# Kernel tuning notes

Measured on AMD Instinct MI355X. Metric: run time of the kernel, lower is better.

## Reference

```python
import jax, jax.numpy as jnp
import numpy as np

B, T, TRAIN = 4, 2048, 1536
D, H, L, FF, V = 512, 8, 12, 2048, 100
DH = D // H
ROPE_BASE = 100000.0


def layer_norm(x, g, b, eps=1e-5):
    mu = jnp.mean(x, axis=-1, keepdims=True)
    var = jnp.mean(jnp.square(x - mu), axis=-1, keepdims=True)
    return (x - mu) * jax.lax.rsqrt(var + eps) * g + b


def rope_cos_sin(t, dh):
    inv_freq = 1.0 / (ROPE_BASE ** (jnp.arange(0, dh, 2, dtype=jnp.float32) / dh))  # (dh/2,)
    ang = jnp.arange(t, dtype=jnp.float32)[:, None] * inv_freq[None, :]  # (T, dh/2)
    return jnp.cos(ang), jnp.sin(ang)


def apply_rope_interleaved(x, cos, sin):
    # x: (B, T, H, DH); interleaved pairs (x0,x1),(x2,x3),...
    x1, x2 = x[..., 0::2], x[..., 1::2]
    c, s = cos[None, :, None, :], sin[None, :, None, :]
    r1 = x1 * c - x2 * s
    r2 = x1 * s + x2 * c
    return jnp.stack([r1, r2], axis=-1).reshape(x.shape)


def setup_inputs() -> dict:
    key = jax.random.key(0)
    ks = jax.random.split(key, 20)
    sc = 0.02
    inp = {
        'R': jax.random.normal(ks[0], (B, T, D), jnp.float32),
        'y_train': jax.random.randint(ks[1], (B, TRAIN), 0, V),
        'emb': jax.random.normal(ks[2], (V, D), jnp.float32) * sc,
        'Wqkv': jax.random.normal(ks[3], (L, D, 3 * D), jnp.float32) * sc,
        'bqkv': jnp.zeros((L, 3 * D), jnp.float32),
        'Wo': jax.random.normal(ks[4], (L, D, D), jnp.float32) * sc,
        'bo': jnp.zeros((L, D), jnp.float32),
        'ln1_g': jnp.ones((L, D), jnp.float32),
        'ln1_b': jnp.zeros((L, D), jnp.float32),
        'ln2_g': jnp.ones((L, D), jnp.float32),
        'ln2_b': jnp.zeros((L, D), jnp.float32),
        'W1': jax.random.normal(ks[5], (L, D, FF), jnp.float32) * sc,
        'b1': jnp.zeros((L, FF), jnp.float32),
        'W2': jax.random.normal(ks[6], (L, FF, D), jnp.float32) * sc,
        'b2': jnp.zeros((L, D), jnp.float32),
        'pW1': jax.random.normal(ks[7], (D, 2 * D), jnp.float32) * sc,
        'pb1': jnp.zeros((2 * D,), jnp.float32),
        'pW2': jax.random.normal(ks[8], (2 * D, V), jnp.float32) * sc,
        'pb2': jnp.zeros((V,), jnp.float32),
    }
    return inp


def icl_forward(R, y_train, emb, Wqkv, bqkv, Wo, bo, ln1_g, ln1_b, ln2_g, ln2_b, W1, b1, W2, b2, pW1, pb1, pW2, pb2):
    b, t, d = R.shape
    train = y_train.shape[1]
    # label embedding: train rows get emb[y], test rows get zeros
    y_emb = jnp.concatenate([emb[y_train], jnp.zeros((b, t - train, d), R.dtype)], axis=1)
    rep = R + y_emb
    # ICL mask: column j visible iff j < train or j == i
    idx = jnp.arange(t)
    allowed = (idx[None, :] < train) | (idx[:, None] == idx[None, :])
    mask = jnp.where(allowed, 0.0, -jnp.inf).astype(R.dtype)  # (T, T)
    cos, sin = rope_cos_sin(t, DH)
    scale = 1.0 / jnp.sqrt(jnp.asarray(DH, R.dtype))

    def block(x, p):
        wqkv, bq, wo, bob, g1, be1, g2, be2, w1, bb1, w2, bb2 = p
        h = layer_norm(x, g1, be1)
        qkv = h @ wqkv + bq  # (B,T,3D)
        q, k, v = jnp.split(qkv, 3, axis=-1)
        q = q.reshape(b, t, H, DH)
        k = k.reshape(b, t, H, DH)
        v = v.reshape(b, t, H, DH)
        q = apply_rope_interleaved(q, cos, sin)
        k = apply_rope_interleaved(k, cos, sin)
        scores = jnp.einsum('bthd,bshd->bhts', q, k) * scale + mask
        attn = jax.nn.softmax(scores, axis=-1)
        o = jnp.einsum('bhts,bshd->bthd', attn, v).reshape(b, t, d)
        x = x + o @ wo + bob
        h2 = layer_norm(x, g2, be2)
        x = x + jax.nn.gelu(h2 @ w1 + bb1) @ w2 + bb2
        return x, None

    rep, _ = jax.lax.scan(block, rep, (Wqkv, bqkv, Wo, bo, ln1_g, ln1_b, ln2_g, ln2_b, W1, b1, W2, b2))
    test = rep[:, train:, :]
    logits = jax.nn.gelu(test @ pW1 + pb1) @ pW2 + pb2  # (B, test, V)
    return logits


def reference(R, y_train, emb, Wqkv, bqkv, Wo, bo, ln1_g, ln1_b, ln2_g, ln2_b, W1, b1, W2, b2, pW1, pb1, pW2, pb2):
    return icl_forward(R, y_train, emb, Wqkv, bqkv, Wo, bo, ln1_g, ln1_b, ln2_g, ln2_b, W1, b1, W2, b2, pW1, pb1, pW2, pb2)
```

## Files before the change

kernel.cpp:

```cpp
#include <hip/hip_runtime.h>
#include <hip/hip_bf16.h>

#define BB 4
#define TT 2048
#define TRAIN 1536
#define DD 512
#define HH 8
#define LL 12
#define FFD 2048
#define VV 100
#define DH 64
#define NT (BB*TT)
#define NTEST (BB*(TT-TRAIN))

typedef __bf16 bf16x8 __attribute__((ext_vector_type(8)));
typedef float  f32x4  __attribute__((ext_vector_type(4)));

#define GLDS16(g, l) __builtin_amdgcn_global_load_lds( \
    (const __attribute__((address_space(1))) void*)(g), \
    (__attribute__((address_space(3))) void*)(l), 16, 0, 0)

__global__ __launch_bounds__(256) void emb_add(const float* __restrict__ R,
                                               const int* __restrict__ y,
                                               const float* __restrict__ emb,
                                               float* __restrict__ rep) {
    int idx = blockIdx.x * 256 + threadIdx.x;
    int d = idx & 511;
    int n = idx >> 9;
    int t = n & (TT - 1);
    int b = n >> 11;
    float val = R[idx];
    if (t < TRAIN) {
        int tok = y[b * TRAIN + t];
        val += emb[(size_t)tok * DD + d];
    }
    rep[idx] = val;
}

__global__ __launch_bounds__(256) void ln_wave(const float* __restrict__ x,
                                               const float* __restrict__ g,
                                               const float* __restrict__ bta,
                                               __bf16* __restrict__ out) {
    int row = blockIdx.x * 4 + (threadIdx.x >> 6);
    int lane = threadIdx.x & 63;
    const float* xr = x + (size_t)row * DD + lane * 8;
    float4 a = *(const float4*)xr;
    float4 c = *(const float4*)(xr + 4);
    float s  = a.x + a.y + a.z + a.w + c.x + c.y + c.z + c.w;
    float sq = a.x*a.x + a.y*a.y + a.z*a.z + a.w*a.w + c.x*c.x + c.y*c.y + c.z*c.z + c.w*c.w;
#pragma unroll
    for (int off = 1; off < 64; off <<= 1) {
        s  += __shfl_xor(s, off);
        sq += __shfl_xor(sq, off);
    }
    float mu  = s * (1.0f / DD);
    float var = sq * (1.0f / DD) - mu * mu;
    float inv = rsqrtf(var + 1e-5f);
    const float* gp = g + lane * 8;
    const float* bp = bta + lane * 8;
    float4 g0 = *(const float4*)gp, g1 = *(const float4*)(gp + 4);
    float4 b0 = *(const float4*)bp, b1 = *(const float4*)(bp + 4);
    __bf16 o8[8];
    o8[0] = (__bf16)((a.x - mu) * inv * g0.x + b0.x);
    o8[1] = (__bf16)((a.y - mu) * inv * g0.y + b0.y);
    o8[2] = (__bf16)((a.z - mu) * inv * g0.z + b0.z);
    o8[3] = (__bf16)((a.w - mu) * inv * g0.w + b0.w);
    o8[4] = (__bf16)((c.x - mu) * inv * g1.x + b1.x);
    o8[5] = (__bf16)((c.y - mu) * inv * g1.y + b1.y);
    o8[6] = (__bf16)((c.z - mu) * inv * g1.z + b1.z);
    o8[7] = (__bf16)((c.w - mu) * inv * g1.w + b1.w);
    *(uint4*)(out + (size_t)row * DD + lane * 8) = *(uint4*)o8;
}

__global__ __launch_bounds__(256) void rope_tab(float* __restrict__ ctab, float* __restrict__ stab) {
    int idx = blockIdx.x * 256 + threadIdx.x;
    int p = idx & 31, t = idx >> 5;
    double freq = exp(-((double)(2 * p) / 64.0) * log(100000.0));
    double ang = (double)t * freq;
    ctab[idx] = (float)cos(ang);
    stab[idx] = (float)sin(ang);
}

__global__ __launch_bounds__(256) void rope_vt(const __bf16* __restrict__ qkv,
                                               const float* __restrict__ ctab,
                                               const float* __restrict__ stab,
                                               __bf16* __restrict__ qo,
                                               __bf16* __restrict__ ko,
                                               __bf16* __restrict__ vt) {
    int bh = blockIdx.y; int b = bh >> 3, h = bh & 7;
    int t0 = blockIdx.x * 64;
    __shared__ __bf16 tile[64][72];
    int tid = threadIdx.x;
    {
        int r = tid >> 2, cg = (tid & 3) * 16;
        const __bf16* src = qkv + (size_t)(b * TT + t0 + r) * (3 * DD) + 2 * DD + h * DH + cg;
        *(uint4*)&tile[r][cg]     = *(const uint4*)&src[0];
        *(uint4*)&tile[r][cg + 8] = *(const uint4*)&src[8];
    }
#pragma unroll
    for (int c = 0; c < 8; ++c) {
        int pidx = c * 256 + tid;
        int tl = pidx >> 5, p = pidx & 31;
        int t = t0 + tl;
        const __bf16* base = qkv + (size_t)(b * TT + t) * (3 * DD) + h * DH;
        float co = ctab[t * 32 + p], si = stab[t * 32 + p];
        float x1 = (float)base[2 * p],       x2 = (float)base[2 * p + 1];
        float k1 = (float)base[DD + 2 * p], k2 = (float)base[DD + 2 * p + 1];
        size_t ob = ((size_t)bh * TT + t) * DH;
        qo[ob + 2 * p]     = (__bf16)(x1 * co - x2 * si);
        qo[ob + 2 * p + 1] = (__bf16)(x1 * si + x2 * co);
        ko[ob + 2 * p]     = (__bf16)(k1 * co - k2 * si);
        ko[ob + 2 * p + 1] = (__bf16)(k1 * si + k2 * co);
    }
    __syncthreads();
    {
        int dh = tid >> 2, tg = (tid & 3) * 16;
        __bf16 outv[16];
#pragma unroll
        for (int j = 0; j < 16; ++j) outv[j] = tile[tg + j][dh];
        __bf16* dst = vt + ((size_t)bh * DH + dh) * TT + t0 + tg;
        *(uint4*)&dst[0] = *(uint4*)&outv[0];
        *(uint4*)&dst[8] = *(uint4*)&outv[8];
    }
}

#define NCH (TRAIN/128)
#define PSE 136

__global__ __launch_bounds__(512, 2) void attn_mfma(const __bf16* __restrict__ q,
                                                    const __bf16* __restrict__ k,
                                                    const __bf16* __restrict__ vt,
                                                    __bf16* __restrict__ obuf) {
    __shared__ __align__(16) __bf16 Kb[2][128 * 64];
    __shared__ __align__(16) __bf16 Vb[64 * 128];
    __shared__ __align__(16) __bf16 Pb[256 * PSE];
    __shared__ float sself[256];

    const int tid = threadIdx.x;
    const int bh = blockIdx.y;
    const int b = bh >> 3, hh = bh & 7;
    const size_t kbase = (size_t)bh * TT * DH;
    const int t0q = blockIdx.x * 256;
    const int w = tid >> 6;
    const int lane = tid & 63;
    const int l16 = lane & 15;
    const int quad = lane >> 4;
    const int x7 = l16 & 7;

    bf16x8 qa[2][2];
#pragma unroll
    for (int mi = 0; mi < 2; ++mi)
#pragma unroll
        for (int ks = 0; ks < 2; ++ks) {
            const __bf16* qg = q + kbase + (size_t)(t0q + w * 32 + mi * 16 + l16) * DH + ks * 32 + quad * 8;
            uint4 u = *(const uint4*)qg;
            const __bf16* pb = (const __bf16*)&u;
            bf16x8 vq;
#pragma unroll
            for (int j = 0; j < 8; ++j) vq[j] = (__bf16)((float)pb[j] * 0.125f);
            qa[mi][ks] = vq;
        }

    const int krl = lane >> 3, ksl = lane & 7;
    const int vrl = lane >> 4, vsl = lane & 15;

    f32x4 oa[2][4] = {};
    float lsum[2] = {0.f, 0.f};

    {
        const __bf16* g = k + kbase;
#pragma unroll
        for (int c = 0; c < 2; ++c) {
            int rb = w * 2 + c;
            GLDS16(g + (size_t)(rb * 8 + krl) * DH + ((ksl ^ krl) * 8), &Kb[0][rb * 512]);
        }
    }

    for (int ci = 0; ci < NCH; ++ci) {
        __syncthreads();
        {
#pragma unroll
            for (int c = 0; c < 2; ++c) {
                int rb = w * 2 + c;
                int dh = rb * 4 + vrl;
                GLDS16(vt + kbase + (size_t)dh * TT + ci * 128 + ((vsl ^ (dh & 7)) * 8), &Vb[rb * 512]);
            }
        }

        const __bf16* kc = Kb[ci & 1];
        f32x4 acc[2][8] = {};
        __builtin_amdgcn_s_setprio(1);
#pragma unroll
        for (int ks = 0; ks < 2; ++ks) {
            bf16x8 kf[8];
#pragma unroll
            for (int ni = 0; ni < 8; ++ni)
                kf[ni] = *(const bf16x8*)&kc[(ni * 16 + l16) * 64 + (((ks * 4 + quad) ^ x7) * 8)];
#pragma unroll
            for (int ni = 0; ni < 8; ++ni) {
                acc[0][ni] = __builtin_amdgcn_mfma_f32_16x16x32_bf16(kf[ni], qa[0][ks], acc[0][ni], 0, 0, 0);
                acc[1][ni] = __builtin_amdgcn_mfma_f32_16x16x32_bf16(kf[ni], qa[1][ks], acc[1][ni], 0, 0, 0);
            }
        }
        __builtin_amdgcn_s_setprio(0);

#pragma unroll
        for (int mi = 0; mi < 2; ++mi) {
            float rs = 0.f;
#pragma unroll
            for (int ni = 0; ni < 8; ++ni) {
                float p0 = __expf(acc[mi][ni][0]);
                float p1 = __expf(acc[mi][ni][1]);
                float p2 = __expf(acc[mi][ni][2]);
                float p3 = __expf(acc[mi][ni][3]);
                rs += (p0 + p1) + (p2 + p3);
                __bf16 p4[4] = {(__bf16)p0, (__bf16)p1, (__bf16)p2, (__bf16)p3};
                *(uint2*)&Pb[(w * 32 + mi * 16 + l16) * PSE + ni * 16 + quad * 4] = *(const uint2*)p4;
            }
            rs += __shfl_xor(rs, 16);
            rs += __shfl_xor(rs, 32);
            lsum[mi] += rs;
        }

        __syncthreads();
        if (ci + 1 < NCH) {
            const __bf16* g = k + kbase + (size_t)((ci + 1) * 128) * DH;
            __bf16* dst = Kb[(ci + 1) & 1];
#pragma unroll
            for (int c = 0; c < 2; ++c) {
                int rb = w * 2 + c;
                GLDS16(g + (size_t)(rb * 8 + krl) * DH + ((ksl ^ krl) * 8), dst + rb * 512);
            }
        }

        __builtin_amdgcn_s_setprio(1);
#pragma unroll
        for (int ks = 0; ks < 4; ++ks) {
            bf16x8 vf[4];
#pragma unroll
            for (int ni = 0; ni < 4; ++ni)
                vf[ni] = *(const bf16x8*)&Vb[(ni * 16 + l16) * 128 + (((ks * 4 + quad) ^ x7) * 8)];
            bf16x8 pa0 = *(const bf16x8*)&Pb[(w * 32 + l16) * PSE + ks * 32 + quad * 8];
            bf16x8 pa1 = *(const bf16x8*)&Pb[(w * 32 + 16 + l16) * PSE + ks * 32 + quad * 8];
#pragma unroll
            for (int ni = 0; ni < 4; ++ni) {
                oa[0][ni] = __builtin_amdgcn_mfma_f32_16x16x32_bf16(pa0, vf[ni], oa[0][ni], 0, 0, 0);
                oa[1][ni] = __builtin_amdgcn_mfma_f32_16x16x32_bf16(pa1, vf[ni], oa[1][ni], 0, 0, 0);
            }
        }
        __builtin_amdgcn_s_setprio(0);
    }

    float lr[2][4];
#pragma unroll
    for (int mi = 0; mi < 2; ++mi)
#pragma unroll
        for (int r = 0; r < 4; ++r)
            lr[mi][r] = __shfl(lsum[mi], quad * 4 + r);

    if (t0q >= TRAIN) {
        __bf16* selfV = &Kb[0][0];
        __syncthreads();
        {
            int dh = tid >> 3, c0 = (tid & 7) * 32;
            const __bf16* vg = vt + kbase + (size_t)dh * TT + t0q + c0;
#pragma unroll
            for (int u = 0; u < 4; ++u)
                *(uint4*)&selfV[dh * 256 + c0 + u * 8] = *(const uint4*)&vg[u * 8];
            int row = tid >> 1, hf = tid & 1;
            const __bf16* qp = q + kbase + (size_t)(t0q + row) * DH + hf * 32;
            const __bf16* kp = k + kbase + (size_t)(t0q + row) * DH + hf * 32;
            float dacc = 0.f;
#pragma unroll
            for (int u = 0; u < 4; ++u) {
                uint4 uq = *(const uint4*)&qp[u * 8];
                uint4 uk = *(const uint4*)&kp[u * 8];
                const __bf16* pq = (const __bf16*)&uq;
                const __bf16* pk = (const __bf16*)&uk;
#pragma unroll
                for (int j = 0; j < 8; ++j) dacc += (float)pq[j] * (float)pk[j];
            }
            dacc += __shfl_xor(dacc, 1);
            sself[row] = dacc * 0.125f;
        }
        __syncthreads();
#pragma unroll
        for (int mi = 0; mi < 2; ++mi)
#pragma unroll
            for (int r = 0; r < 4; ++r) {
                int qr = w * 32 + mi * 16 + quad * 4 + r;
                float pp = __expf(sself[qr]);
                lr[mi][r] += pp;
#pragma unroll
                for (int ni = 0; ni < 4; ++ni)
                    oa[mi][ni][r] += pp * (float)selfV[(ni * 16 + l16) * 256 + qr];
            }
    }

#pragma unroll
    for (int mi = 0; mi < 2; ++mi)
#pragma unroll
        for (int r = 0; r < 4; ++r) {
            float inv = 1.f / lr[mi][r];
            int trow = t0q + w * 32 + mi * 16 + quad * 4 + r;
            __bf16* op = obuf + ((size_t)(b * TT) + trow) * DD + hh * 64;
#pragma unroll
            for (int ni = 0; ni < 4; ++ni)
                op[ni * 16 + l16] = (__bf16)(oa[mi][ni][r] * inv);
        }
}

__global__ __launch_bounds__(256) void transpose_pad(const float* __restrict__ src,
                                                     __bf16* __restrict__ dst,
                                                     int K, int N) {
    __shared__ __bf16 t[32][33];
    int n0 = blockIdx.x * 32, k0 = blockIdx.y * 32;
    int tx = threadIdx.x & 31, ty = threadIdx.x >> 5;
#pragma unroll
    for (int i = 0; i < 4; ++i) {
        int nn = n0 + tx;
        t[ty + i * 8][tx] = (nn < N) ? (__bf16)src[(size_t)(k0 + ty + i * 8) * N + nn] : (__bf16)0.f;
    }
    __syncthreads();
#pragma unroll
    for (int i = 0; i < 4; ++i) {
        dst[(size_t)(n0 + ty + i * 8) * K + k0 + tx] = t[tx][ty + i * 8];
    }
}

__global__ __launch_bounds__(256) void transpose_all(const float* __restrict__ s0,
                                                     const float* __restrict__ s1,
                                                     const float* __restrict__ s2,
                                                     const float* __restrict__ s3,
                                                     __bf16* __restrict__ d0, __bf16* __restrict__ d1,
                                                     __bf16* __restrict__ d2, __bf16* __restrict__ d3) {
    int i = blockIdx.x;
    const float* src; __bf16* dst; int K, N, tx, ty;
    if (i < 768)       { src = s0; dst = d0; K = 512;  N = 1536; int j = i;        tx = j % 48; ty = j / 48; }
    else if (i < 1024) { src = s1; dst = d1; K = 512;  N = 512;  int j = i - 768;  tx = j % 16; ty = j / 16; }
    else if (i < 2048) { src = s2; dst = d2; K = 512;  N = 2048; int j = i - 1024; tx = j % 64; ty = j / 64; }
    else               { src = s3; dst = d3; K = 2048; N = 512;  int j = i - 2048; tx = j % 16; ty = j / 16; }
    __shared__ __bf16 t[32][33];
    int n0 = tx * 32, k0 = ty * 32;
    int lx = threadIdx.x & 31, ly = threadIdx.x >> 5;
#pragma unroll
    for (int c = 0; c < 4; ++c)
        t[ly + c * 8][lx] = (__bf16)src[(size_t)(k0 + ly + c * 8) * N + n0 + lx];
    __syncthreads();
#pragma unroll
    for (int c = 0; c < 4; ++c)
        dst[(size_t)(n0 + ly + c * 8) * K + k0 + lx] = t[lx][ly + c * 8];
}

template <int EP, int TN>
__global__ __launch_bounds__(256) void gemm_bt(const __bf16* __restrict__ A,
                                               const __bf16* __restrict__ Bt,
                                               const float* __restrict__ bias,
                                               float* __restrict__ resid,
                                               __bf16* __restrict__ Cout,
                                               int M, int N, int K) {
    constexpr int NI = TN / 32;
    __shared__ __align__(16) __bf16 As[2][128 * 32];
    __shared__ __align__(16) __bf16 Bs[2][TN * 32];
    const int tid = threadIdx.x;
    const int m0 = blockIdx.x * 128;
    const int n0 = blockIdx.y * TN;
    const int lane = tid & 63;
    const int w = tid >> 6;
    const int wm = (w >> 1) * 64, wn = (w & 1) * (TN / 2);
    const int lrow = lane & 15;
    const int kq = (lane >> 4) * 8;

    f32x4 acc[4][NI] = {};

    const int srA = w * 32 + (lane >> 2);
    const int srB = w * (TN / 4) + (lane >> 2);
    const int scol = (lane & 3) * 8;
    const __bf16* gA = A  + (size_t)(m0 + srA) * K + scol;
    const __bf16* gB = Bt + (size_t)(n0 + srB) * K + scol;
    __bf16* lA0 = &As[0][(w * 32) * 32];
    __bf16* lA0b = lA0 + 16 * 32;
    __bf16* lA1 = &As[1][(w * 32) * 32];
    __bf16* lA1b = lA1 + 16 * 32;
    __bf16* lB0 = &Bs[0][(w * (TN / 4)) * 32];
    __bf16* lB1 = &Bs[1][(w * (TN / 4)) * 32];

    const int nk = K >> 6;
    for (int kt = 0; kt < nk; ++kt) {
        const int k0 = kt << 6;
        GLDS16(gA + k0,            lA0);
        GLDS16(gA + 16 * K + k0,   lA0b);
        GLDS16(gA + k0 + 32,       lA1);
        GLDS16(gA + 16 * K + k0 + 32, lA1b);
        GLDS16(gB + k0,            lB0);
        GLDS16(gB + k0 + 32,       lB1);
        if constexpr (TN == 128) {
            GLDS16(gB + 16 * K + k0,      lB0 + 16 * 32);
            GLDS16(gB + 16 * K + k0 + 32, lB1 + 16 * 32);
        }
        __syncthreads();
#pragma unroll
        for (int ps = 0; ps < 2; ++ps) {
            bf16x8 afr[4], bfr[NI];
#pragma unroll
            for (int i = 0; i < 4; ++i)
                afr[i] = *(const bf16x8*)&As[ps][(wm + i * 16 + lrow) * 32 + kq];
#pragma unroll
            for (int i = 0; i < NI; ++i)
                bfr[i] = *(const bf16x8*)&Bs[ps][(wn + i * 16 + lrow) * 32 + kq];
#pragma unroll
            for (int mi = 0; mi < 4; ++mi)
#pragma unroll
                for (int ni = 0; ni < NI; ++ni)
                    acc[mi][ni] = __builtin_amdgcn_mfma_f32_16x16x32_bf16(afr[mi], bfr[ni], acc[mi][ni], 0, 0, 0);
        }
        __syncthreads();
    }

    const int crow = (lane >> 4) * 4;
    const int ccol = lane & 15;
#pragma unroll
    for (int mi = 0; mi < 4; ++mi) {
#pragma unroll
        for (int ni = 0; ni < NI; ++ni) {
            int gn = n0 + wn + ni * 16 + ccol;
            float bv = bias[gn];
#pragma unroll
            for (int r = 0; r < 4; ++r) {
                int gm = m0 + wm + mi * 16 + crow + r;
                float vvv = acc[mi][ni][r] + bv;
                if constexpr (EP == 1) {
                    float x = vvv;
                    vvv = x / (1.f + __expf(-1.5957691216f * (x + 0.044715f * x * x * x)));
                }
                if constexpr (EP == 2) {
                    resid[(size_t)gm * N + gn] += vvv;
                } else if constexpr (EP == 4) {
                    if (gn < VV) resid[(size_t)gm * VV + gn] = vvv;
                } else {
                    Cout[(size_t)gm * N + gn] = (__bf16)vvv;
                }
            }
        }
    }
}

__global__ __launch_bounds__(256) void cast_test(const float* __restrict__ rep, __bf16* __restrict__ testb) {
    int idx = blockIdx.x * 256 + threadIdx.x;
    int d = idx & 511;
    int i = idx >> 9;
    int ttk = i & 511;
    int b = i >> 9;
    testb[idx] = (__bf16)rep[(size_t)(b * TT + TRAIN + ttk) * DD + d];
}

__global__ void pad_bias(const float* __restrict__ pb2, float* __restrict__ pb2p) {
    int t = threadIdx.x;
    if (t < 128) pb2p[t] = (t < VV) ? pb2[t] : 0.f;
}

extern "C" void kernel_launch(void* const* d_in, const int* in_sizes, int n_in,
                              void* d_out, int out_size, void* d_ws, size_t ws_size,
                              hipStream_t stream) {
    const float* R    = (const float*)d_in[0];
    const int*   y    = (const int*)d_in[1];
    const float* emb  = (const float*)d_in[2];
    const float* Wqkv = (const float*)d_in[3];
    const float* bqkv = (const float*)d_in[4];
    const float* Wo   = (const float*)d_in[5];
    const float* bo   = (const float*)d_in[6];
    const float* ln1g = (const float*)d_in[7];
    const float* ln1b = (const float*)d_in[8];
    const float* ln2g = (const float*)d_in[9];
    const float* ln2b = (const float*)d_in[10];
    const float* W1   = (const float*)d_in[11];
    const float* b1   = (const float*)d_in[12];
    const float* W2   = (const float*)d_in[13];
    const float* b2   = (const float*)d_in[14];
    const float* pW1  = (const float*)d_in[15];
    const float* pb1  = (const float*)d_in[16];
    const float* pW2  = (const float*)d_in[17];
    const float* pb2  = (const float*)d_in[18];

    char* p = (char*)d_ws;
    float* rep    = (float*)p;  p += (size_t)NT * DD * 4;
    __bf16* hbuf  = (__bf16*)p; p += (size_t)NT * DD * 2;
    __bf16* qkv   = (__bf16*)p;
    __bf16* ffb   = qkv;        p += (size_t)NT * FFD * 2;
    __bf16* qb    = (__bf16*)p; p += (size_t)NT * DD * 2;
    __bf16* kb    = (__bf16*)p; p += (size_t)NT * DD * 2;
    __bf16* vtb   = (__bf16*)p; p += (size_t)NT * DD * 2;
    __bf16* obuf  = (__bf16*)p; p += (size_t)NT * DD * 2;
    __bf16* wqkvT = (__bf16*)p; p += (size_t)1536 * 512 * 2;
    __bf16* woT   = (__bf16*)p; p += (size_t)512 * 512 * 2;
    __bf16* w1T   = (__bf16*)p; p += (size_t)2048 * 512 * 2;
    __bf16* w2T   = (__bf16*)p; p += (size_t)512 * 2048 * 2;
    float* ctab   = (float*)p;  p += (size_t)TT * 32 * 4;
    float* stab   = (float*)p;  p += (size_t)TT * 32 * 4;
    float* pb2p   = (float*)p;  p += 512;
    __bf16* testb = hbuf;
    __bf16* hb    = obuf;

    emb_add<<<NT * DD / 256, 256, 0, stream>>>(R, y, emb, rep);
    rope_tab<<<TT * 32 / 256, 256, 0, stream>>>(ctab, stab);

    for (int l = 0; l < LL; ++l) {
        ln_wave<<<NT / 4, 256, 0, stream>>>(rep, ln1g + l * DD, ln1b + l * DD, hbuf);
        transpose_all<<<3072, 256, 0, stream>>>(Wqkv + (size_t)l * DD * 3 * DD, Wo + (size_t)l * DD * DD,
                                                W1 + (size_t)l * DD * FFD, W2 + (size_t)l * FFD * DD,
                                                wqkvT, woT, w1T, w2T);
        gemm_bt<0, 128><<<dim3(NT / 128, 1536 / 128), 256, 0, stream>>>(hbuf, wqkvT, bqkv + l * 3 * DD, nullptr, qkv, NT, 3 * DD, DD);
        rope_vt<<<dim3(TT / 64, BB * HH), 256, 0, stream>>>(qkv, ctab, stab, qb, kb, vtb);
        attn_mfma<<<dim3(TT / 256, BB * HH), 512, 0, stream>>>(qb, kb, vtb, obuf);
        gemm_bt<2, 64><<<dim3(NT / 128, 512 / 64), 256, 0, stream>>>(obuf, woT, bo + l * DD, rep, nullptr, NT, DD, DD);
        ln_wave<<<NT / 4, 256, 0, stream>>>(rep, ln2g + l * DD, ln2b + l * DD, hbuf);
        gemm_bt<1, 128><<<dim3(NT / 128, FFD / 128), 256, 0, stream>>>(hbuf, w1T, b1 + l * FFD, nullptr, ffb, NT, FFD, DD);
        gemm_bt<2, 64><<<dim3(NT / 128, 512 / 64), 256, 0, stream>>>(ffb, w2T, b2 + l * DD, rep, nullptr, NT, DD, FFD);
    }

    cast_test<<<NTEST * DD / 256, 256, 0, stream>>>(rep, testb);
    transpose_pad<<<dim3(1024 / 32, 512 / 32), 256, 0, stream>>>(pW1, w1T, DD, 2 * DD);
    gemm_bt<1, 64><<<dim3(NTEST / 128, 1024 / 64), 256, 0, stream>>>(testb, w1T, pb1, nullptr, hb, NTEST, 2 * DD, DD);
    pad_bias<<<1, 128, 0, stream>>>(pb2, pb2p);
    transpose_pad<<<dim3(128 / 32, 1024 / 32), 256, 0, stream>>>(pW2, w2T, 2 * DD, VV);
    gemm_bt<4, 128><<<dim3(NTEST / 128, 1), 256, 0, stream>>>(hb, w2T, pb2p, (float*)d_out, nullptr, NTEST, 128, 2 * DD);
}
```

Before: 2.337 ms.

## Keep attention probabilities in registers via permlane swaps and remap blocks per XCD

The attention kernel now packs exp scores to bf16 with v_cvt_pk_bf16_f32 and rearranges them across lanes with permlane swaps, so the P tile is fed straight into the PV MFMA instead of going through a large shared-memory buffer. Query tiles shrink from 256 to 128 rows with 256-thread blocks, which lowers LDS use and raises the block count. Both the attention and GEMM kernels remap linear block IDs so that blocks sharing the same head or row panel land on the same XCD, aiming to improve L2 reuse. The cost is a fragile register layout that depends on MFMA operand ordering, and K/V tiles are loaded by fewer threads per block.

```diff
diff --git a/kernel.cpp b/kernel.cpp
--- a/kernel.cpp
+++ b/kernel.cpp
@@ -15,6 +15,7 @@
 
 typedef __bf16 bf16x8 __attribute__((ext_vector_type(8)));
 typedef float  f32x4  __attribute__((ext_vector_type(4)));
+typedef unsigned int u32x4 __attribute__((ext_vector_type(4)));
 
 #define GLDS16(g, l) __builtin_amdgcn_global_load_lds( \
     (const __attribute__((address_space(1))) void*)(g), \
@@ -125,22 +126,22 @@
 }
 
 #define NCH (TRAIN/128)
-#define PSE 136
-
-__global__ __launch_bounds__(512, 2) void attn_mfma(const __bf16* __restrict__ q,
+
+__global__ __launch_bounds__(256, 2) void attn_mfma(const __bf16* __restrict__ q,
                                                     const __bf16* __restrict__ k,
                                                     const __bf16* __restrict__ vt,
                                                     __bf16* __restrict__ obuf) {
     __shared__ __align__(16) __bf16 Kb[2][128 * 64];
     __shared__ __align__(16) __bf16 Vb[64 * 128];
-    __shared__ __align__(16) __bf16 Pb[256 * PSE];
-    __shared__ float sself[256];
+    __shared__ float sself[128];
 
     const int tid = threadIdx.x;
-    const int bh = blockIdx.y;
+    const int lin = blockIdx.x;
+    const int xcd = lin & 7, sblk = lin >> 3;
+    const int bh = xcd * 4 + (sblk & 3);
+    const int t0q = (sblk >> 2) * 128;
     const int b = bh >> 3, hh = bh & 7;
     const size_t kbase = (size_t)bh * TT * DH;
-    const int t0q = blockIdx.x * 256;
     const int w = tid >> 6;
     const int lane = tid & 63;
     const int l16 = lane & 15;
@@ -170,21 +171,19 @@
     {
         const __bf16* g = k + kbase;
 #pragma unroll
-        for (int c = 0; c < 2; ++c) {
-            int rb = w * 2 + c;
+        for (int c = 0; c < 4; ++c) {
+            int rb = w * 4 + c;
             GLDS16(g + (size_t)(rb * 8 + krl) * DH + ((ksl ^ krl) * 8), &Kb[0][rb * 512]);
         }
     }
 
     for (int ci = 0; ci < NCH; ++ci) {
         __syncthreads();
-        {
-#pragma unroll
-            for (int c = 0; c < 2; ++c) {
-                int rb = w * 2 + c;
-                int dh = rb * 4 + vrl;
-                GLDS16(vt + kbase + (size_t)dh * TT + ci * 128 + ((vsl ^ (dh & 7)) * 8), &Vb[rb * 512]);
-            }
+#pragma unroll
+        for (int c = 0; c < 4; ++c) {
+            int rb = w * 4 + c;
+            int dh = rb * 4 + vrl;
+            GLDS16(vt + kbase + (size_t)dh * TT + ci * 128 + ((vsl ^ (dh & 7)) * 8), &Vb[rb * 512]);
         }
 
         const __bf16* kc = Kb[ci & 1];
@@ -204,8 +203,10 @@
         }
         __builtin_amdgcn_s_setprio(0);
 
+        u32x4 pa[2][4];
 #pragma unroll
         for (int mi = 0; mi < 2; ++mi) {
+            unsigned int pk[8][2];
             float rs = 0.f;
 #pragma unroll
             for (int ni = 0; ni < 8; ++ni) {
@@ -214,12 +215,22 @@
                 float p2 = __expf(acc[mi][ni][2]);
                 float p3 = __expf(acc[mi][ni][3]);
                 rs += (p0 + p1) + (p2 + p3);
-                __bf16 p4[4] = {(__bf16)p0, (__bf16)p1, (__bf16)p2, (__bf16)p3};
-                *(uint2*)&Pb[(w * 32 + mi * 16 + l16) * PSE + ni * 16 + quad * 4] = *(const uint2*)p4;
+                asm("v_cvt_pk_bf16_f32 %0, %1, %2" : "=v"(pk[ni][0]) : "v"(p0), "v"(p1));
+                asm("v_cvt_pk_bf16_f32 %0, %1, %2" : "=v"(pk[ni][1]) : "v"(p2), "v"(p3));
             }
             rs += __shfl_xor(rs, 16);
             rs += __shfl_xor(rs, 32);
             lsum[mi] += rs;
+#pragma unroll
+            for (int ks = 0; ks < 4; ++ks)
+#pragma unroll
+                for (int rr = 0; rr < 2; ++rr) {
+                    unsigned int A = pk[2 * ks][rr], Bv = pk[2 * ks + 1][rr];
+                    asm("v_permlane32_swap_b32 %0, %1" : "+v"(A), "+v"(Bv));
+                    asm("v_permlane16_swap_b32 %0, %1" : "+v"(A), "+v"(Bv));
+                    pa[mi][ks][rr]     = A;
+                    pa[mi][ks][rr + 2] = Bv;
+                }
         }
 
         __syncthreads();
@@ -227,8 +238,8 @@
             const __bf16* g = k + kbase + (size_t)((ci + 1) * 128) * DH;
             __bf16* dst = Kb[(ci + 1) & 1];
 #pragma unroll
-            for (int c = 0; c < 2; ++c) {
-                int rb = w * 2 + c;
+            for (int c = 0; c < 4; ++c) {
+                int rb = w * 4 + c;
                 GLDS16(g + (size_t)(rb * 8 + krl) * DH + ((ksl ^ krl) * 8), dst + rb * 512);
             }
         }
@@ -240,8 +251,9 @@
 #pragma unroll
             for (int ni = 0; ni < 4; ++ni)
                 vf[ni] = *(const bf16x8*)&Vb[(ni * 16 + l16) * 128 + (((ks * 4 + quad) ^ x7) * 8)];
-            bf16x8 pa0 = *(const bf16x8*)&Pb[(w * 32 + l16) * PSE + ks * 32 + quad * 8];
-            bf16x8 pa1 = *(const bf16x8*)&Pb[(w * 32 + 16 + l16) * PSE + ks * 32 + quad * 8];
+            bf16x8 pa0, pa1;
+            { u32x4 t = pa[0][ks]; __builtin_memcpy(&pa0, &t, 16); }
+            { u32x4 t = pa[1][ks]; __builtin_memcpy(&pa1, &t, 16); }
 #pragma unroll
             for (int ni = 0; ni < 4; ++ni) {
                 oa[0][ni] = __builtin_amdgcn_mfma_f32_16x16x32_bf16(pa0, vf[ni], oa[0][ni], 0, 0, 0);
@@ -259,14 +271,13 @@
             lr[mi][r] = __shfl(lsum[mi], quad * 4 + r);
 
     if (t0q >= TRAIN) {
-        __bf16* selfV = &Kb[0][0];
         __syncthreads();
         {
-            int dh = tid >> 3, c0 = (tid & 7) * 32;
-            const __bf16* vg = vt + kbase + (size_t)dh * TT + t0q + c0;
+            int dh = tid >> 2, cg = (tid & 3) * 32;
+            const __bf16* vg = vt + kbase + (size_t)dh * TT + t0q + cg;
 #pragma unroll
             for (int u = 0; u < 4; ++u)
-                *(uint4*)&selfV[dh * 256 + c0 + u * 8] = *(const uint4*)&vg[u * 8];
+                *(uint4*)&Vb[dh * 128 + cg + u * 8] = *(const uint4*)&vg[u * 8];
             int row = tid >> 1, hf = tid & 1;
             const __bf16* qp = q + kbase + (size_t)(t0q + row) * DH + hf * 32;
             const __bf16* kp = k + kbase + (size_t)(t0q + row) * DH + hf * 32;
@@ -276,9 +287,9 @@
                 uint4 uq = *(const uint4*)&qp[u * 8];
                 uint4 uk = *(const uint4*)&kp[u * 8];
                 const __bf16* pq = (const __bf16*)&uq;
-                const __bf16* pk = (const __bf16*)&uk;
-#pragma unroll
-                for (int j = 0; j < 8; ++j) dacc += (float)pq[j] * (float)pk[j];
+                const __bf16* pk2 = (const __bf16*)&uk;
+#pragma unroll
+                for (int j = 0; j < 8; ++j) dacc += (float)pq[j] * (float)pk2[j];
             }
             dacc += __shfl_xor(dacc, 1);
             sself[row] = dacc * 0.125f;
@@ -293,7 +304,7 @@
                 lr[mi][r] += pp;
 #pragma unroll
                 for (int ni = 0; ni < 4; ++ni)
-                    oa[mi][ni][r] += pp * (float)selfV[(ni * 16 + l16) * 256 + qr];
+                    oa[mi][ni][r] += pp * (float)Vb[(ni * 16 + l16) * 128 + qr];
             }
     }
 
@@ -363,8 +374,14 @@
     __shared__ __align__(16) __bf16 As[2][128 * 32];
     __shared__ __align__(16) __bf16 Bs[2][TN * 32];
     const int tid = threadIdx.x;
-    const int m0 = blockIdx.x * 128;
-    const int n0 = blockIdx.y * TN;
+    const int gx = gridDim.x;
+    const int linb = blockIdx.x + gx * blockIdx.y;
+    const int xs = gx >> 3;
+    const int xcd = linb & 7, sb = linb >> 3;
+    const int bx = xcd * xs + (sb % xs);
+    const int by = sb / xs;
+    const int m0 = bx * 128;
+    const int n0 = by * TN;
     const int lane = tid & 63;
     const int w = tid >> 6;
     const int wm = (w >> 1) * 64, wn = (w & 1) * (TN / 2);
@@ -511,7 +528,7 @@
                                                 wqkvT, woT, w1T, w2T);
         gemm_bt<0, 128><<<dim3(NT / 128, 1536 / 128), 256, 0, stream>>>(hbuf, wqkvT, bqkv + l * 3 * DD, nullptr, qkv, NT, 3 * DD, DD);
         rope_vt<<<dim3(TT / 64, BB * HH), 256, 0, stream>>>(qkv, ctab, stab, qb, kb, vtb);
-        attn_mfma<<<dim3(TT / 256, BB * HH), 512, 0, stream>>>(qb, kb, vtb, obuf);
+        attn_mfma<<<dim3(512), 256, 0, stream>>>(qb, kb, vtb, obuf);
         gemm_bt<2, 64><<<dim3(NT / 128, 512 / 64), 256, 0, stream>>>(obuf, woT, bo + l * DD, rep, nullptr, NT, DD, DD);
         ln_wave<<<NT / 4, 256, 0, stream>>>(rep, ln2g + l * DD, ln2b + l * DD, hbuf);
         gemm_bt<1, 128><<<dim3(NT / 128, FFD / 128), 256, 0, stream>>>(hbuf, w1T, b1 + l * FFD, nullptr, ffb, NT, FFD, DD);
```

Result: no change. 2.298 ms (-1.7%).
